# Performance work log

Hardware: AMD Instinct MI355X
Metric: run time of the kernel (lower is better)

## Reference

```python
import jax, jax.numpy as jnp
import numpy as np

B, S, F, D, K = 4096, 64, 8, 64, 16  # batch_size, seq_len, input_size, d_model, knns


def setup_inputs() -> dict:
    key = jax.random.key(0)
    ks = jax.random.split(key, 3)
    return {
        "x": jax.random.normal(ks[0], (B, S, F), jnp.float32),
        "W_emb": jax.random.normal(ks[1], (F, D), jnp.float32) / np.sqrt(F),
        "b_emb": jnp.zeros((D,), jnp.float32),
        "W_proj": jax.random.normal(ks[2], (D, F), jnp.float32) / np.sqrt(D),
        "b_proj": jnp.zeros((F,), jnp.float32),
    }


def reference(x, W_emb, b_emb, W_proj, b_proj):
    # enc_embedding
    x_enc = x @ W_emb + b_emb                       # [B,S,D]
    x_re = x_enc.reshape(B, S * D)                  # flatten per sample
    # batch self-similarity
    attn = jnp.einsum('bl,cl->bc', x_re, x_re) / np.sqrt(D * S)
    diag = jnp.eye(B, dtype=bool)
    attn = jnp.where(diag, -jnp.inf, attn)
    scores = jax.nn.softmax(attn, axis=-1)          # [B,B]
    # einsum('bd,bc->bd', x_re, scores) == x_re * scores.sum(-1)
    x_rec = x_re * jnp.sum(scores, axis=-1, keepdims=True)
    x_rec = x_rec.reshape(B, S, D)
    x_rec_proj = x_rec @ W_proj + b_proj            # [B,S,F]
    # top-k neighbor gather
    _, top_idx = jax.lax.top_k(scores, K)           # [B,K] int32
    gathered = x_rec_proj[top_idx]                  # [B,K,S,F]
    diff_1 = jnp.mean(jnp.diff(gathered, axis=1) ** 2)
    diff_2 = jnp.mean(jnp.diff(gathered, axis=2) ** 2)
    loss = jnp.mean((x_rec_proj - x) ** 2) + diff_1 + diff_2  # var == 2
    return loss, x_rec_proj
```

## Files before the change

kernel.cpp:

```cpp
#include <hip/hip_runtime.h>
#include <math.h>

#define NB 4096
#define NS 64
#define NF 8
#define ND 64
#define KL 512
#define NK 16

typedef _Float16 half8 __attribute__((ext_vector_type(8)));
typedef float    f32x4 __attribute__((ext_vector_type(4)));

#define GLD16(src, dst) \
  __builtin_amdgcn_global_load_lds((const __attribute__((address_space(1))) void*)(src), \
                                   (__attribute__((address_space(3))) void*)(dst), 16, 0, 0)

#define WAITVM(N) asm volatile("s_waitcnt vmcnt(" #N ")" ::: "memory")

__device__ __forceinline__ unsigned f32key(float v, int col) {
    const unsigned u = __float_as_uint(v);
    const unsigned s = ((int)u < 0) ? ~u : (u | 0x80000000u);
    return (s & 0xFFFFF000u) | (unsigned)(4095 - col);
}

#define UPD2(M1, M2, K) { const unsigned k_ = (K); \
    if (k_ > M1) { M2 = M1; M1 = k_; } else if (k_ > M2) M2 = k_; }

__device__ __forceinline__ float blk_reduce(float v, float* red) {
    #pragma unroll
    for (int o = 32; o > 0; o >>= 1) v += __shfl_down(v, o, 64);
    const int t = threadIdx.x;
    __syncthreads();
    if ((t & 63) == 0) red[t >> 6] = v;
    __syncthreads();
    float r = 0.f;
    if (t == 0) r = red[0] + red[1] + red[2] + red[3];
    return r;
}

__global__ __launch_bounds__(256) void prep_kernel(
    const float* __restrict__ x, const float* __restrict__ Wemb,
    const float* __restrict__ bemb, const float* __restrict__ Wp,
    const float* __restrict__ bp,
    _Float16* __restrict__ X16, _Float16* __restrict__ Y16,
    float* __restrict__ proj, float* __restrict__ r, double* __restrict__ p1)
{
    __shared__ float sWe[512], sWp[512], sbe[64], sbp[8];
    __shared__ float sG[64], sM[64], su[8], sc[8];
    __shared__ float red[4];
    const int t = threadIdx.x, lane = t & 63, w = t >> 6;
    sWe[t] = Wemb[t]; sWe[t + 256] = Wemb[t + 256];
    sWp[t] = Wp[t];   sWp[t + 256] = Wp[t + 256];
    if (t < 64) sbe[t] = bemb[t];
    if (t < 8)  sbp[t] = bp[t];
    __syncthreads();
    if (t < 64) {
        const int f = t >> 3, f2 = t & 7;
        float g = 0.f, m = 0.f;
        #pragma unroll
        for (int d = 0; d < ND; ++d) {
            g += sWe[f * ND + d] * sWe[f2 * ND + d];
            m += sWe[f * ND + d] * sWp[d * NF + f2];
        }
        sG[t] = g; sM[t] = m;
    }
    if (t < 8) {
        float uu = 0.f, cc = 0.f;
        #pragma unroll
        for (int d = 0; d < ND; ++d) {
            uu += sWe[t * ND + d] * sbe[d];
            cc += sbe[d] * sWp[d * NF + t];
        }
        su[t] = uu; sc[t] = cc + sbp[t];
    }
    __syncthreads();

    const int b = blockIdx.x * 4 + w;
    const size_t base = (size_t)b * KL + lane * 8;
    const f32x4 x0 = *(const f32x4*)&x[base];
    const f32x4 x1 = *(const f32x4*)&x[base + 4];
    float xv[8] = {x0[0], x0[1], x0[2], x0[3], x1[0], x1[1], x1[2], x1[3]};
    float yv[8], pv[8];
    #pragma unroll
    for (int f2 = 0; f2 < 8; ++f2) { yv[f2] = 0.f; pv[f2] = sc[f2]; }
    #pragma unroll
    for (int f = 0; f < 8; ++f)
        #pragma unroll
        for (int f2 = 0; f2 < 8; ++f2) {
            yv[f2] += xv[f] * sG[f * 8 + f2];
            pv[f2] += xv[f] * sM[f * 8 + f2];
        }
    half8 hx, hy;
    #pragma unroll
    for (int j = 0; j < 8; ++j) { hx[j] = (_Float16)xv[j]; hy[j] = (_Float16)yv[j]; }
    *(half8*)&X16[base] = hx;
    *(half8*)&Y16[base] = hy;
    *(f32x4*)&proj[base] = (f32x4){pv[0], pv[1], pv[2], pv[3]};
    *(f32x4*)&proj[base + 4] = (f32x4){pv[4], pv[5], pv[6], pv[7]};
    float rv = 0.f;
    #pragma unroll
    for (int f = 0; f < 8; ++f) rv += xv[f] * su[f];
    #pragma unroll
    for (int o = 32; o > 0; o >>= 1) rv += __shfl_down(rv, o, 64);
    if (lane == 0) r[b] = rv;
    float s1 = 0.f;
    #pragma unroll
    for (int j = 0; j < 8; ++j) { const float d = pv[j] - xv[j]; s1 += d * d; }
    const float tot = blk_reduce(s1, red);
    if (t == 0) p1[blockIdx.x] = (double)tot;
}

__global__ __launch_bounds__(256) void attn_gemm_kernel(
    const _Float16* __restrict__ Xf, const _Float16* __restrict__ Yf,
    const float* __restrict__ rvec, unsigned* __restrict__ cand)
{
    __shared__ __align__(16) char smem_raw[49152];
    _Float16* smem = (_Float16*)smem_raw;

    const int t = threadIdx.x;
    const int lane = t & 63, wid = t >> 6;

    const int bid0 = blockIdx.x;
    const int bid = (bid0 & 7) * 256 + (bid0 >> 3);
    const int it = bid >> 6, jt = bid & 63;
    const int i0 = it * 128, j0 = jt * 64;

    f32x4 acc[2][4];
    #pragma unroll
    for (int m = 0; m < 2; ++m)
        #pragma unroll
        for (int n = 0; n < 4; ++n) acc[m][n] = (f32x4){0.f, 0.f, 0.f, 0.f};

    const int lrow = lane & 15, g = lane >> 4;
    const int ksw = (g ^ ((lrow >> 1) & 3)) * 8;

    const int rA0 = t >> 2,         cA0 = t & 3;
    const int rA1 = (t + 256) >> 2;
    const int csA0 = (cA0 ^ ((rA0 >> 1) & 3)) * 8;
    const int csA1 = (cA0 ^ ((rA1 >> 1) & 3)) * 8;
    const _Float16* pA0 = Xf + (size_t)(i0 + rA0) * KL + csA0;
    const _Float16* pA1 = Xf + (size_t)(i0 + rA1) * KL + csA1;
    const _Float16* pB  = Yf + (size_t)(j0 + rA0) * KL + csA0;
    _Float16* dA0 = smem + t * 8;
    _Float16* dA1 = smem + (t + 256) * 8;
    _Float16* dB  = smem + 4096 + t * 8;

#define STG(BUF, KH) { \
    GLD16(pA0 + (KH), dA0 + (BUF) * 6144); \
    GLD16(pA1 + (KH), dA1 + (BUF) * 6144); \
    GLD16(pB  + (KH), dB  + (BUF) * 6144); }

    const int roA = wid * 1024 + lrow * 32 + ksw;
    const int roB = lrow * 32 + ksw;

#define COMPUTE(BUF) { \
    const _Float16* sA = smem + (BUF) * 6144 + roA; \
    const _Float16* sB = smem + (BUF) * 6144 + 4096 + roB; \
    half8 fa[2], fb[4]; \
    _Pragma("unroll") \
    for (int m = 0; m < 2; ++m) fa[m] = *(const half8*)&sA[m * 512]; \
    _Pragma("unroll") \
    for (int n = 0; n < 4; ++n) fb[n] = *(const half8*)&sB[n * 512]; \
    _Pragma("unroll") \
    for (int m = 0; m < 2; ++m) \
        _Pragma("unroll") \
        for (int n = 0; n < 4; ++n) \
            acc[m][n] = __builtin_amdgcn_mfma_f32_16x16x32_f16(fa[m], fb[n], acc[m][n], 0, 0, 0); }

    STG(0, 0); STG(1, 32); STG(2, 64);
    pA0 += 96; pA1 += 96; pB += 96;
    #pragma unroll 1
    for (int io = 0; io < 3; ++io) {
        WAITVM(6); __builtin_amdgcn_s_barrier(); STG(3, 0);  COMPUTE(0);
        WAITVM(6); __builtin_amdgcn_s_barrier(); STG(0, 32); COMPUTE(1);
        WAITVM(6); __builtin_amdgcn_s_barrier(); STG(1, 64); COMPUTE(2);
        WAITVM(6); __builtin_amdgcn_s_barrier(); STG(2, 96); COMPUTE(3);
        pA0 += 128; pA1 += 128; pB += 128;
    }
    WAITVM(6); __builtin_amdgcn_s_barrier(); STG(3, 0); COMPUTE(0);
    WAITVM(6); __builtin_amdgcn_s_barrier(); COMPUTE(1);
    WAITVM(3); __builtin_amdgcn_s_barrier(); COMPUTE(2);
    WAITVM(0); __builtin_amdgcn_s_barrier(); COMPUTE(3);
#undef STG
#undef COMPUTE

    float rj[4];
    #pragma unroll
    for (int n = 0; n < 4; ++n) rj[n] = rvec[j0 + n * 16 + lrow];

    uint2* dp = (uint2*)smem_raw;
    __syncthreads();

    #pragma unroll
    for (int m = 0; m < 2; ++m)
        #pragma unroll
        for (int rr = 0; rr < 4; ++rr) {
            const int rl = wid * 32 + m * 16 + g * 4 + rr;
            const int i  = i0 + rl;
            unsigned m1 = 0u, m2 = 0u;
            #pragma unroll
            for (int n = 0; n < 4; ++n) {
                const int j = j0 + n * 16 + lrow;
                unsigned key = f32key(acc[m][n][rr] + rj[n], j);
                if (i == j) key = 0u;
                UPD2(m1, m2, key)
            }
            uint2 pr; pr.x = m1; pr.y = m2;
            dp[rl * 17 + lrow] = pr;
        }

    __syncthreads();

    if (t < 128) {
        unsigned m1 = 0u, m2 = 0u;
        #pragma unroll
        for (int l = 0; l < 16; ++l) {
            const uint2 pr = dp[t * 17 + l];
            UPD2(m1, m2, pr.x) UPD2(m1, m2, pr.y)
        }
        uint2 st; st.x = m1; st.y = m2;
        *(uint2*)(cand + (size_t)(i0 + t) * 128 + (size_t)jt * 2) = st;
    }
}

__global__ __launch_bounds__(256) void topk_diffs_kernel(
    const unsigned* __restrict__ cand, const float* __restrict__ proj,
    double* __restrict__ p2, double* __restrict__ p3)
{
    __shared__ double bs1[4], bs2[4];
    const int t = threadIdx.x, lane = t & 63, w = t >> 6;
    const int b = blockIdx.x * 4 + w;
    const uint2 kk = *(const uint2*)(cand + (size_t)b * 128 + lane * 2);
    unsigned k0 = kk.x, k1 = kk.y;

    float s1 = 0.f, s2 = 0.f;
    float prev[8];

    for (int k = 0; k < NK; ++k) {
        unsigned bv = k0 > k1 ? k0 : k1;
        #pragma unroll
        for (int o = 1; o <= 32; o <<= 1)
            bv = max(bv, (unsigned)__shfl_xor((int)bv, o, 64));
        const int idx = 4095 - (int)(bv & 0xFFFu);

        const float* pp = proj + (size_t)idx * 512 + lane * 8;
        const f32x4 a0 = *(const f32x4*)pp;
        const f32x4 a1 = *(const f32x4*)(pp + 4);
        float cur[8] = {a0[0], a0[1], a0[2], a0[3], a1[0], a1[1], a1[2], a1[3]};
        if (k) {
            #pragma unroll
            for (int j = 0; j < 8; ++j) { const float d = cur[j] - prev[j]; s1 += d * d; }
        }
        if (lane < 63) {
            const f32x4 n0 = *(const f32x4*)(pp + 8);
            const f32x4 n1 = *(const f32x4*)(pp + 12);
            const float nxt[8] = {n0[0], n0[1], n0[2], n0[3], n1[0], n1[1], n1[2], n1[3]};
            #pragma unroll
            for (int j = 0; j < 8; ++j) { const float d = nxt[j] - cur[j]; s2 += d * d; }
        }
        #pragma unroll
        for (int j = 0; j < 8; ++j) prev[j] = cur[j];

        if (k0 == bv) k0 = 0u;
        if (k1 == bv) k1 = 0u;
    }

    #pragma unroll
    for (int o = 32; o > 0; o >>= 1) { s1 += __shfl_down(s1, o, 64); s2 += __shfl_down(s2, o, 64); }
    if (lane == 0) { bs1[w] = (double)s1; bs2[w] = (double)s2; }
    __syncthreads();
    if (t == 0) {
        p2[blockIdx.x] = bs1[0] + bs1[1] + bs1[2] + bs1[3];
        p3[blockIdx.x] = bs2[0] + bs2[1] + bs2[2] + bs2[3];
    }
}

__global__ __launch_bounds__(256) void finalize_kernel(
    const double* __restrict__ p1, const double* __restrict__ p2,
    const double* __restrict__ p3, float* __restrict__ out)
{
    __shared__ double dred[4];
    const int t = threadIdx.x, lane = t & 63, w = t >> 6;
    double v = 0.0;
    for (int i = t; i < 1024; i += 256)
        v += p1[i] * (1.0 / 2097152.0)
           + p2[i] * (1.0 / 31457280.0)
           + p3[i] * (1.0 / 33030144.0);
    #pragma unroll
    for (int o = 32; o > 0; o >>= 1) v += __shfl_down(v, o, 64);
    if (lane == 0) dred[w] = v;
    __syncthreads();
    if (t == 0) out[0] = (float)(dred[0] + dred[1] + dred[2] + dred[3]);
}

extern "C" void kernel_launch(void* const* d_in, const int* in_sizes, int n_in,
                              void* d_out, int out_size, void* d_ws, size_t ws_size,
                              hipStream_t stream) {
    const float* x    = (const float*)d_in[0];
    const float* Wemb = (const float*)d_in[1];
    const float* bemb = (const float*)d_in[2];
    const float* Wp   = (const float*)d_in[3];
    const float* bp   = (const float*)d_in[4];
    float* out  = (float*)d_out;
    float* proj = out + 1;

    char* ws = (char*)d_ws;
    _Float16* X16 = (_Float16*)ws;
    _Float16* Y16 = (_Float16*)(ws + ((size_t)4 << 20));
    unsigned* cand = (unsigned*)(ws + ((size_t)8 << 20));
    float*  rvec  = (float*)(ws + ((size_t)10 << 20));
    double* p1    = (double*)(ws + ((size_t)10 << 20) + 65536);
    double* p2    = p1 + 1024;
    double* p3    = p2 + 1024;

    prep_kernel<<<NB / 4, 256, 0, stream>>>(x, Wemb, bemb, Wp, bp, X16, Y16, proj, rvec, p1);
    attn_gemm_kernel<<<2048, 256, 0, stream>>>(X16, Y16, rvec, cand);
    topk_diffs_kernel<<<NB / 4, 256, 0, stream>>>(cand, proj, p2, p3);
    finalize_kernel<<<1, 256, 0, stream>>>(p1, p2, p3, out);
}
```

Baseline: 66.46 us.

## Widen GEMM K-step to 64 with triple buffering and XCD-aware tile mapping

The attention GEMM now stages 64-wide K slices per buffer (three buffers instead of four 32-wide ones), using an 8-way XOR swizzle over 128-byte rows. Each stage issues two MFMA K-substeps, which halves the number of barriers and wait points in the K loop. The block-to-tile mapping is changed so each XCD handles a contiguous 2D sub-grid of tiles, aiming for better L2 reuse of the A and B rows. LDS grows to 72KB per block, which may reduce how many blocks can be resident on a CU.

```diff
diff --git a/kernel.cpp b/kernel.cpp
--- a/kernel.cpp
+++ b/kernel.cpp
@@ -114,15 +114,15 @@
     const _Float16* __restrict__ Xf, const _Float16* __restrict__ Yf,
     const float* __restrict__ rvec, unsigned* __restrict__ cand)
 {
-    __shared__ __align__(16) char smem_raw[49152];
+    __shared__ __align__(16) char smem_raw[73728];
     _Float16* smem = (_Float16*)smem_raw;
 
     const int t = threadIdx.x;
     const int lane = t & 63, wid = t >> 6;
 
-    const int bid0 = blockIdx.x;
-    const int bid = (bid0 & 7) * 256 + (bid0 >> 3);
-    const int it = bid >> 6, jt = bid & 63;
+    const int xcd = blockIdx.x & 7, q = blockIdx.x >> 3;
+    const int it = (xcd >> 1) * 8 + (q >> 5);
+    const int jt = (xcd & 1) * 32 + (q & 31);
     const int i0 = it * 128, j0 = jt * 64;
 
     f32x4 acc[2][4];
@@ -132,57 +132,73 @@
         for (int n = 0; n < 4; ++n) acc[m][n] = (f32x4){0.f, 0.f, 0.f, 0.f};
 
     const int lrow = lane & 15, g = lane >> 4;
-    const int ksw = (g ^ ((lrow >> 1) & 3)) * 8;
-
-    const int rA0 = t >> 2,         cA0 = t & 3;
-    const int rA1 = (t + 256) >> 2;
-    const int csA0 = (cA0 ^ ((rA0 >> 1) & 3)) * 8;
-    const int csA1 = (cA0 ^ ((rA1 >> 1) & 3)) * 8;
-    const _Float16* pA0 = Xf + (size_t)(i0 + rA0) * KL + csA0;
-    const _Float16* pA1 = Xf + (size_t)(i0 + rA1) * KL + csA1;
-    const _Float16* pB  = Yf + (size_t)(j0 + rA0) * KL + csA0;
-    _Float16* dA0 = smem + t * 8;
-    _Float16* dA1 = smem + (t + 256) * 8;
-    _Float16* dB  = smem + 4096 + t * 8;
+
+    const int idA0 = t,       rA0 = idA0 >> 3, cA0s = ((idA0 & 7) ^ (rA0 & 7)) * 8;
+    const int idA1 = t + 256, rA1 = idA1 >> 3, cA1s = ((idA1 & 7) ^ (rA1 & 7)) * 8;
+    const int idA2 = t + 512, rA2 = idA2 >> 3, cA2s = ((idA2 & 7) ^ (rA2 & 7)) * 8;
+    const int idA3 = t + 768, rA3 = idA3 >> 3, cA3s = ((idA3 & 7) ^ (rA3 & 7)) * 8;
+    const int idB0 = t,       rB0 = idB0 >> 3, cB0s = ((idB0 & 7) ^ (rB0 & 7)) * 8;
+    const int idB1 = t + 256, rB1 = idB1 >> 3, cB1s = ((idB1 & 7) ^ (rB1 & 7)) * 8;
+    const _Float16* pA0 = Xf + (size_t)(i0 + rA0) * KL + cA0s;
+    const _Float16* pA1 = Xf + (size_t)(i0 + rA1) * KL + cA1s;
+    const _Float16* pA2 = Xf + (size_t)(i0 + rA2) * KL + cA2s;
+    const _Float16* pA3 = Xf + (size_t)(i0 + rA3) * KL + cA3s;
+    const _Float16* pB0 = Yf + (size_t)(j0 + rB0) * KL + cB0s;
+    const _Float16* pB1 = Yf + (size_t)(j0 + rB1) * KL + cB1s;
+    _Float16* dA0 = smem + idA0 * 8;
+    _Float16* dA1 = smem + idA1 * 8;
+    _Float16* dA2 = smem + idA2 * 8;
+    _Float16* dA3 = smem + idA3 * 8;
+    _Float16* dB0 = smem + 8192 + idB0 * 8;
+    _Float16* dB1 = smem + 8192 + idB1 * 8;
 
 #define STG(BUF, KH) { \
-    GLD16(pA0 + (KH), dA0 + (BUF) * 6144); \
-    GLD16(pA1 + (KH), dA1 + (BUF) * 6144); \
-    GLD16(pB  + (KH), dB  + (BUF) * 6144); }
-
-    const int roA = wid * 1024 + lrow * 32 + ksw;
-    const int roB = lrow * 32 + ksw;
+    GLD16(pA0 + (KH), dA0 + (BUF) * 12288); \
+    GLD16(pA1 + (KH), dA1 + (BUF) * 12288); \
+    GLD16(pA2 + (KH), dA2 + (BUF) * 12288); \
+    GLD16(pA3 + (KH), dA3 + (BUF) * 12288); \
+    GLD16(pB0 + (KH), dB0 + (BUF) * 12288); \
+    GLD16(pB1 + (KH), dB1 + (BUF) * 12288); }
+
+    const int swz0 = (g ^ (lrow & 7)) * 8;
+    const int swz1 = ((4 + g) ^ (lrow & 7)) * 8;
+    const int roA = (wid * 32 + lrow) * 64;
+    const int roB = lrow * 64;
 
 #define COMPUTE(BUF) { \
-    const _Float16* sA = smem + (BUF) * 6144 + roA; \
-    const _Float16* sB = smem + (BUF) * 6144 + 4096 + roB; \
-    half8 fa[2], fb[4]; \
+    const _Float16* sA = smem + (BUF) * 12288 + roA; \
+    const _Float16* sB = smem + (BUF) * 12288 + 8192 + roB; \
     _Pragma("unroll") \
-    for (int m = 0; m < 2; ++m) fa[m] = *(const half8*)&sA[m * 512]; \
-    _Pragma("unroll") \
-    for (int n = 0; n < 4; ++n) fb[n] = *(const half8*)&sB[n * 512]; \
-    _Pragma("unroll") \
-    for (int m = 0; m < 2; ++m) \
+    for (int ks = 0; ks < 2; ++ks) { \
+        const int sw = ks ? swz1 : swz0; \
+        half8 fa[2], fb[4]; \
         _Pragma("unroll") \
-        for (int n = 0; n < 4; ++n) \
-            acc[m][n] = __builtin_amdgcn_mfma_f32_16x16x32_f16(fa[m], fb[n], acc[m][n], 0, 0, 0); }
-
-    STG(0, 0); STG(1, 32); STG(2, 64);
-    pA0 += 96; pA1 += 96; pB += 96;
+        for (int m = 0; m < 2; ++m) fa[m] = *(const half8*)&sA[m * 1024 + sw]; \
+        _Pragma("unroll") \
+        for (int n = 0; n < 4; ++n) fb[n] = *(const half8*)&sB[n * 1024 + sw]; \
+        _Pragma("unroll") \
+        for (int m = 0; m < 2; ++m) \
+            _Pragma("unroll") \
+            for (int n = 0; n < 4; ++n) \
+                acc[m][n] = __builtin_amdgcn_mfma_f32_16x16x32_f16(fa[m], fb[n], acc[m][n], 0, 0, 0); \
+    } }
+
+#define BUMP(NH) { pA0 += NH; pA1 += NH; pA2 += NH; pA3 += NH; pB0 += NH; pB1 += NH; }
+
+    STG(0, 0); STG(1, 64);
+    BUMP(128)
     #pragma unroll 1
-    for (int io = 0; io < 3; ++io) {
-        WAITVM(6); __builtin_amdgcn_s_barrier(); STG(3, 0);  COMPUTE(0);
-        WAITVM(6); __builtin_amdgcn_s_barrier(); STG(0, 32); COMPUTE(1);
-        WAITVM(6); __builtin_amdgcn_s_barrier(); STG(1, 64); COMPUTE(2);
-        WAITVM(6); __builtin_amdgcn_s_barrier(); STG(2, 96); COMPUTE(3);
-        pA0 += 128; pA1 += 128; pB += 128;
-    }
-    WAITVM(6); __builtin_amdgcn_s_barrier(); STG(3, 0); COMPUTE(0);
-    WAITVM(6); __builtin_amdgcn_s_barrier(); COMPUTE(1);
-    WAITVM(3); __builtin_amdgcn_s_barrier(); COMPUTE(2);
-    WAITVM(0); __builtin_amdgcn_s_barrier(); COMPUTE(3);
+    for (int io = 0; io < 2; ++io) {
+        WAITVM(6); __builtin_amdgcn_s_barrier(); STG(2, 0);   COMPUTE(0);
+        WAITVM(6); __builtin_amdgcn_s_barrier(); STG(0, 64);  COMPUTE(1);
+        WAITVM(6); __builtin_amdgcn_s_barrier(); STG(1, 128); COMPUTE(2);
+        BUMP(192)
+    }
+    WAITVM(6); __builtin_amdgcn_s_barrier(); COMPUTE(0);
+    WAITVM(0); __builtin_amdgcn_s_barrier(); COMPUTE(1);
 #undef STG
 #undef COMPUTE
+#undef BUMP
 
     float rj[4];
     #pragma unroll
```

Measured after the change: 66.04 us, median of 2. About the same (-0.6%).
